# Optimization experiments

Hardware: AMD Instinct MI355X
Metric: run time of the kernel (lower is better)

## Reference

```python
import jax, jax.numpy as jnp
import numpy as np

SCALE = 2
KSIZE = 3
EPS = 0.2  # damping constant in 1/(grad^2 + 0.2)


def _unfold_patches(x, k):
    """x: [B, C, H, W] -> [B, C, k*k, H, W], zero-padded, row-major window order
    (matches torch.nn.functional.unfold channel ordering)."""
    B, C, H, W = x.shape
    p = k // 2
    xp = jnp.pad(x, ((0, 0), (0, 0), (p, p), (p, p)))
    return jnp.stack(
        [xp[:, :, i:i + H, j:j + W] for i in range(k) for j in range(k)], axis=2
    )


def setup_inputs() -> dict:
    key = jax.random.key(0)
    x = jax.random.normal(key, (4, 128, 128, 128), dtype=jnp.float32)
    return {"x": x}


def reference(x):
    B, C, H, W = x.shape
    k, s = KSIZE, SCALE
    k2 = k * k

    # channel-mean map [B, 1, H, W]
    mean = jnp.mean(x, axis=1, keepdims=True)

    # local gradients of the mean map: unfold(mean) - mean  -> [B, k2, H, W]
    grad = _unfold_patches(mean, k)[:, 0] - mean
    grad = 1.0 / (grad * grad + EPS)

    # nearest-neighbor upsample by s (F.interpolate default mode='nearest')
    up = jnp.repeat(jnp.repeat(grad, s, axis=2), s, axis=3)  # [B, k2, Hs, Ws]
    kernels = jax.nn.softmax(up, axis=1)

    # CARAFE content-aware reassembly (group=1):
    # output pixel (i, j) gathers the kxk neighborhood of source pixel
    # (i//s, j//s) of x and reduces it with kernels[:, :, i, j].
    patches = _unfold_patches(x, k)                 # [B, C, k2, H, W]
    Kr = kernels.reshape(B, k2, H, s, W, s)         # split upsampled grid
    out = jnp.einsum('bkhpwq,bckhw->bchpwq', Kr, patches)
    return out.reshape(B, C, H * s, W * s)
```

## Files before the change

### kernel.cpp

```cpp
#include <hip/hip_runtime.h>

#define NB 4
#define NC 128
#define NH 128
#define NW 128
#define EPSV 0.2f
#define TH 2

typedef float v4f __attribute__((ext_vector_type(4)));

__global__ __launch_bounds__(512) void fused_carafe(const float* __restrict__ x,
                                                    float* __restrict__ out) {
    const int chunk = gridDim.x >> 3;
    const int bid = blockIdx.x;
    const int swz = (bid & 7) * chunk + (bid >> 3);
    const int b  = swz >> 6;
    const int h0 = (swz & 63) * TH;

    __shared__ v4f  partA[4][4][32];
    __shared__ float mrow[4][NW];
    __shared__ float wgt[TH][9][NW];

    const int tid = threadIdx.x;

    {
        const int r  = tid >> 7;
        const int cg = (tid >> 5) & 3;
        const int w4 = tid & 31;
        const int hh = h0 - 1 + r;
        v4f s = {0.f, 0.f, 0.f, 0.f};
        if (hh >= 0 && hh < NH) {
            const v4f* px = (const v4f*)(x + (((size_t)(b * NC + cg * 32)) * NH + hh) * NW) + w4;
            v4f s0 = {0.f,0.f,0.f,0.f}, s1 = {0.f,0.f,0.f,0.f};
            #pragma unroll 8
            for (int c = 0; c < 32; c += 2) {
                s0 += px[(size_t)c * (NH * NW / 4)];
                s1 += px[(size_t)(c + 1) * (NH * NW / 4)];
            }
            s = s0 + s1;
        }
        partA[r][cg][w4] = s;
    }
    __syncthreads();
    if (tid < 128) {
        const int r  = tid >> 5;
        const int w4 = tid & 31;
        v4f s = partA[r][0][w4] + partA[r][1][w4] + partA[r][2][w4] + partA[r][3][w4];
        s *= (1.0f / NC);
        *(v4f*)&mrow[r][4 * w4] = s;
    }
    __syncthreads();

    if (tid < 256) {
        const int r = tid >> 7;
        const int w = tid & 127;
        const float mc = mrow[r + 1][w];
        float v[9];
        float vmax = -1e30f;
        #pragma unroll
        for (int ky = 0; ky < 3; ++ky) {
            #pragma unroll
            for (int kx = -1; kx <= 1; ++kx) {
                const int ww = w + kx;
                const float mp = (ww >= 0 && ww < NW) ? mrow[r + ky][ww] : 0.f;
                const float g = mp - mc;
                const float val = 1.0f / (g * g + EPSV);
                v[ky * 3 + kx + 1] = val;
                vmax = fmaxf(vmax, val);
            }
        }
        float sum = 0.f;
        #pragma unroll
        for (int k = 0; k < 9; ++k) { v[k] = __expf(v[k] - vmax); sum += v[k]; }
        const float rs = 1.0f / sum;
        #pragma unroll
        for (int k = 0; k < 9; ++k) wgt[r][k][w] = v[k] * rs;
    }
    __syncthreads();

    const int wp = tid & 63;
    const int cg_ = tid >> 6;
    const int wa = 2 * wp;

    float wA0[9], wB0[9], wA1[9], wB1[9];
    #pragma unroll
    for (int k = 0; k < 9; ++k) {
        wA0[k] = wgt[0][k][wa];  wB0[k] = wgt[0][k][wa + 1];
        wA1[k] = wgt[1][k][wa];  wB1[k] = wgt[1][k][wa + 1];
    }

    const bool rv0 = (h0 > 0), rv3 = (h0 + 2 < NH);
    const bool tv0 = (wp > 0), tv3 = (wp < 63);

    #pragma unroll 2
    for (int i = 0; i < 16; ++i) {
        const int c = cg_ * 16 + i;
        const float* xc = x + ((size_t)(b * NC + c)) * (NH * NW);

        float a[4][4];
        #pragma unroll
        for (int rr = 0; rr < 4; ++rr) {
            const int hh = h0 - 1 + rr;
            const bool rv = (rr == 0) ? rv0 : ((rr == 3) ? rv3 : true);
            const float* row = xc + hh * NW + wa;
            a[rr][0] = (rv && tv0) ? row[-1] : 0.f;
            a[rr][1] = rv ? row[0] : 0.f;
            a[rr][2] = rv ? row[1] : 0.f;
            a[rr][3] = (rv && tv3) ? row[2] : 0.f;
        }

        float v0a = 0.f, v0b = 0.f, v1a = 0.f, v1b = 0.f;
        #pragma unroll
        for (int ky = 0; ky < 3; ++ky) {
            #pragma unroll
            for (int kx = 0; kx < 3; ++kx) {
                const int k = ky * 3 + kx;
                v0a += wA0[k] * a[ky][kx];
                v0b += wB0[k] * a[ky][kx + 1];
                v1a += wA1[k] * a[ky + 1][kx];
                v1b += wB1[k] * a[ky + 1][kx + 1];
            }
        }

        float* o = out + ((size_t)(b * NC + c) * (NH * 2) + 2 * h0) * (NW * 2) + 4 * wp;
        const v4f p0 = {v0a, v0a, v0b, v0b};
        const v4f p1 = {v1a, v1a, v1b, v1b};
        __builtin_nontemporal_store(p0, (v4f*)(o));
        __builtin_nontemporal_store(p0, (v4f*)(o + (NW * 2)));
        __builtin_nontemporal_store(p1, (v4f*)(o + 2 * (NW * 2)));
        __builtin_nontemporal_store(p1, (v4f*)(o + 3 * (NW * 2)));
    }
}

extern "C" void kernel_launch(void* const* d_in, const int* in_sizes, int n_in,
                              void* d_out, int out_size, void* d_ws, size_t ws_size,
                              hipStream_t stream) {
    const float* x = (const float*)d_in[0];
    float* out = (float*)d_out;
    fused_carafe<<<dim3(NB * NH / TH), dim3(512), 0, stream>>>(x, out);
}
```

Before: 33.02 us.

## Split each row-pair block into two width halves with 256-thread blocks

Each block now handles one half of the image width (64 columns plus a halo) for a row pair, doubling the grid to 512 blocks of 256 threads. The channel-mean prologue, softmax weight computation and shared buffers are resized to the half-width tile with halo handling. The center pixel loads in the main loop are merged into a two-float vector load. This spreads work over more blocks for better CU occupancy and balance, at the cost of redundant halo channel reductions and some idle threads in the reduction step.

```diff
diff --git a/kernel.cpp b/kernel.cpp
--- a/kernel.cpp
+++ b/kernel.cpp
@@ -8,61 +8,72 @@
 #define TH 2
 
 typedef float v4f __attribute__((ext_vector_type(4)));
+typedef float v2f __attribute__((ext_vector_type(2)));
 
-__global__ __launch_bounds__(512) void fused_carafe(const float* __restrict__ x,
+__global__ __launch_bounds__(256) void fused_carafe(const float* __restrict__ x,
                                                     float* __restrict__ out) {
     const int chunk = gridDim.x >> 3;
     const int bid = blockIdx.x;
     const int swz = (bid & 7) * chunk + (bid >> 3);
-    const int b  = swz >> 6;
-    const int h0 = (swz & 63) * TH;
+    const int b   = swz >> 7;
+    const int rem = swz & 127;
+    const int h0  = (rem >> 1) * TH;
+    const int hw  = rem & 1;
 
-    __shared__ v4f  partA[4][4][32];
-    __shared__ float mrow[4][NW];
-    __shared__ float wgt[TH][9][NW];
+    __shared__ v4f  partA[4][4][17];
+    __shared__ float mrow[4][68];
+    __shared__ float wgt[TH][9][64];
 
     const int tid = threadIdx.x;
 
     {
-        const int r  = tid >> 7;
-        const int cg = (tid >> 5) & 3;
-        const int w4 = tid & 31;
+        const int r  = tid >> 6;
+        const int cg = (tid >> 4) & 3;
+        const int t  = tid & 15;
         const int hh = h0 - 1 + r;
+        const int w4base = 15 * hw;
         v4f s = {0.f, 0.f, 0.f, 0.f};
+        v4f s2 = {0.f, 0.f, 0.f, 0.f};
         if (hh >= 0 && hh < NH) {
-            const v4f* px = (const v4f*)(x + (((size_t)(b * NC + cg * 32)) * NH + hh) * NW) + w4;
-            v4f s0 = {0.f,0.f,0.f,0.f}, s1 = {0.f,0.f,0.f,0.f};
+            const v4f* px = (const v4f*)(x + (((size_t)(b * NC + cg * 32)) * NH + hh) * NW);
             #pragma unroll 8
-            for (int c = 0; c < 32; c += 2) {
-                s0 += px[(size_t)c * (NH * NW / 4)];
-                s1 += px[(size_t)(c + 1) * (NH * NW / 4)];
+            for (int c = 0; c < 32; ++c)
+                s += px[(size_t)c * (NH * NW / 4) + w4base + t];
+            if (t == 0) {
+                #pragma unroll 8
+                for (int c = 0; c < 32; ++c)
+                    s2 += px[(size_t)c * (NH * NW / 4) + w4base + 16];
             }
-            s = s0 + s1;
         }
-        partA[r][cg][w4] = s;
+        partA[r][cg][t] = s;
+        if (t == 0) partA[r][cg][16] = s2;
     }
     __syncthreads();
-    if (tid < 128) {
-        const int r  = tid >> 5;
-        const int w4 = tid & 31;
-        v4f s = partA[r][0][w4] + partA[r][1][w4] + partA[r][2][w4] + partA[r][3][w4];
+    if (tid < 68) {
+        const int r = tid / 17;
+        const int p = tid % 17;
+        v4f s = partA[r][0][p] + partA[r][1][p] + partA[r][2][p] + partA[r][3][p];
         s *= (1.0f / NC);
-        *(v4f*)&mrow[r][4 * w4] = s;
+        *(v4f*)&mrow[r][4 * p] = s;
     }
     __syncthreads();
 
-    if (tid < 256) {
-        const int r = tid >> 7;
-        const int w = tid & 127;
-        const float mc = mrow[r + 1][w];
+    if (tid < 128) {
+        const int r  = tid >> 6;
+        const int wl = tid & 63;
+        const int wg = 64 * hw + wl;
+        const int lc = wl + 4 * hw;
+        const float mc = mrow[r + 1][lc];
         float v[9];
         float vmax = -1e30f;
         #pragma unroll
         for (int ky = 0; ky < 3; ++ky) {
             #pragma unroll
             for (int kx = -1; kx <= 1; ++kx) {
-                const int ww = w + kx;
-                const float mp = (ww >= 0 && ww < NW) ? mrow[r + ky][ww] : 0.f;
+                const int wwg = wg + kx;
+                const int lw  = lc + kx;
+                const int lwc = lw < 0 ? 0 : (lw > 67 ? 67 : lw);
+                const float mp = (wwg >= 0 && wwg < NW) ? mrow[r + ky][lwc] : 0.f;
                 const float g = mp - mc;
                 const float val = 1.0f / (g * g + EPSV);
                 v[ky * 3 + kx + 1] = val;
@@ -74,23 +85,24 @@
         for (int k = 0; k < 9; ++k) { v[k] = __expf(v[k] - vmax); sum += v[k]; }
         const float rs = 1.0f / sum;
         #pragma unroll
-        for (int k = 0; k < 9; ++k) wgt[r][k][w] = v[k] * rs;
+        for (int k = 0; k < 9; ++k) wgt[r][k][wl] = v[k] * rs;
     }
     __syncthreads();
 
-    const int wp = tid & 63;
-    const int cg_ = tid >> 6;
-    const int wa = 2 * wp;
+    const int wpl = tid & 31;
+    const int cg_ = tid >> 5;
+    const int wl  = 2 * wpl;
+    const int wa  = 64 * hw + wl;
 
     float wA0[9], wB0[9], wA1[9], wB1[9];
     #pragma unroll
     for (int k = 0; k < 9; ++k) {
-        wA0[k] = wgt[0][k][wa];  wB0[k] = wgt[0][k][wa + 1];
-        wA1[k] = wgt[1][k][wa];  wB1[k] = wgt[1][k][wa + 1];
+        wA0[k] = wgt[0][k][wl];  wB0[k] = wgt[0][k][wl + 1];
+        wA1[k] = wgt[1][k][wl];  wB1[k] = wgt[1][k][wl + 1];
     }
 
     const bool rv0 = (h0 > 0), rv3 = (h0 + 2 < NH);
-    const bool tv0 = (wp > 0), tv3 = (wp < 63);
+    const bool tv0 = (wa > 0), tv3 = (wa + 2 < NW);
 
     #pragma unroll 2
     for (int i = 0; i < 16; ++i) {
@@ -103,9 +115,10 @@
             const int hh = h0 - 1 + rr;
             const bool rv = (rr == 0) ? rv0 : ((rr == 3) ? rv3 : true);
             const float* row = xc + hh * NW + wa;
+            const v2f m = rv ? *(const v2f*)row : (v2f){0.f, 0.f};
             a[rr][0] = (rv && tv0) ? row[-1] : 0.f;
-            a[rr][1] = rv ? row[0] : 0.f;
-            a[rr][2] = rv ? row[1] : 0.f;
+            a[rr][1] = m.x;
+            a[rr][2] = m.y;
             a[rr][3] = (rv && tv3) ? row[2] : 0.f;
         }
 
@@ -122,7 +135,8 @@
             }
         }
 
-        float* o = out + ((size_t)(b * NC + c) * (NH * 2) + 2 * h0) * (NW * 2) + 4 * wp;
+        float* o = out + ((size_t)(b * NC + c) * (NH * 2) + 2 * h0) * (NW * 2)
+                       + 128 * hw + 4 * wpl;
         const v4f p0 = {v0a, v0a, v0b, v0b};
         const v4f p1 = {v1a, v1a, v1b, v1b};
         __builtin_nontemporal_store(p0, (v4f*)(o));
@@ -137,5 +151,5 @@
                               hipStream_t stream) {
     const float* x = (const float*)d_in[0];
     float* out = (float*)d_out;
-    fused_carafe<<<dim3(NB * NH / TH), dim3(512), 0, stream>>>(x, out);
+    fused_carafe<<<dim3(NB * NH / TH * 2), dim3(256), 0, stream>>>(x, out);
 }
```

After: 36.52 us. 1.11x slower.
